# Kernel tuning notes

Hardware: AMD Instinct MI355X
Metric: run time of the kernel (lower is better)

The kernel has to match this reference:

```python
import jax, jax.numpy as jnp
import numpy as np

N, H, W, M = 1, 128, 128, 8
IN_CH, STYLE, VDIR, MASK, HID = 64, 128, 3, 680, 256


def setup_inputs() -> dict:
    key = jax.random.key(0)
    ks = iter(jax.random.split(key, 48))

    def rn(shape, scale=1.0):
        return jax.random.normal(next(ks), shape, jnp.float32) * scale

    d = {}
    d["x"] = rn((N, H, W, M, IN_CH))
    d["raydir"] = rn((N, H, W, 1, VDIR))
    d["z"] = rn((N, STYLE))
    d["m"] = jax.random.uniform(next(ks), (N, H, W, M, MASK), jnp.float32)
    d["fc_m_a_w"] = rn((HID, MASK), 1.0 / np.sqrt(MASK))
    d["fc_viewdir_w"] = rn((HID, VDIR), 1.0 / np.sqrt(VDIR))
    d["fc1_w"] = rn((HID, IN_CH), 1.0 / np.sqrt(IN_CH))
    d["fc1_b"] = jnp.zeros((HID,), jnp.float32)
    for name in ["fc2", "fc3", "fc4", "fc6"]:
        d[name + "_w"] = rn((HID, HID), 1.0 / np.sqrt(HID))
        d[name + "_wa"] = rn((HID, STYLE), 1.0 / np.sqrt(STYLE))
        d[name + "_ba"] = jnp.ones((HID,), jnp.float32)
        d[name + "_wb"] = rn((HID, STYLE), 1.0 / np.sqrt(STYLE))
        d[name + "_bb"] = jnp.zeros((HID,), jnp.float32)
    d["fc_sigma_w"] = rn((1, HID), 1.0 / np.sqrt(HID))
    d["fc_sigma_b"] = jnp.zeros((1,), jnp.float32)
    d["fc5_w"] = rn((HID, HID), 1.0 / np.sqrt(HID))
    d["mod5_wa"] = rn((HID, STYLE), 1.0 / np.sqrt(STYLE))
    d["mod5_ba"] = jnp.ones((HID,), jnp.float32)
    d["mod5_wb"] = rn((HID, STYLE), 1.0 / np.sqrt(STYLE))
    d["mod5_bb"] = jnp.zeros((HID,), jnp.float32)
    d["fc_out_c_w"] = rn((3, HID), 1.0 / np.sqrt(HID))
    d["fc_out_c_b"] = jnp.zeros((3,), jnp.float32)
    return d


def _act(v):
    # LeakyReLU(0.2)
    return jnp.where(v >= 0, v, 0.2 * v)


def _modlin(f, z, w, wa, ba, wb, bb):
    # ModLinear with bias=False, mod_bias=True, output_mode=True.
    # Torch materializes per-sample modulated weights w*alpha then baddbmm;
    # mathematically identical to scaling the input: y = (f*alpha) @ w.T + beta.
    alpha = z @ wa.T + ba  # (N, in)
    beta = z @ wb.T + bb   # (N, out)
    y = jnp.einsum('bhwmi,oi->bhwmo', f * alpha[:, None, None, None, :], w)
    return y + beta[:, None, None, None, :]


def reference(x, raydir, z, m, fc_m_a_w, fc_viewdir_w, fc1_w, fc1_b,
              fc2_w, fc2_wa, fc2_ba, fc2_wb, fc2_bb,
              fc3_w, fc3_wa, fc3_ba, fc3_wb, fc3_bb,
              fc4_w, fc4_wa, fc4_ba, fc4_wb, fc4_bb,
              fc_sigma_w, fc_sigma_b, fc5_w,
              mod5_wa, mod5_ba, mod5_wb, mod5_bb,
              fc6_w, fc6_wa, fc6_ba, fc6_wb, fc6_bb,
              fc_out_c_w, fc_out_c_b):
    f = jnp.einsum('bhwmi,oi->bhwmo', x, fc1_w) + fc1_b
    f = f + jnp.einsum('bhwmi,oi->bhwmo', m, fc_m_a_w)  # use_seg branch
    f = _act(f)
    f = _act(_modlin(f, z, fc2_w, fc2_wa, fc2_ba, fc2_wb, fc2_bb))
    f = _act(_modlin(f, z, fc3_w, fc3_wa, fc3_ba, fc3_wb, fc3_bb))
    f = _act(_modlin(f, z, fc4_w, fc4_wa, fc4_ba, fc4_wb, fc4_bb))
    sigma = jnp.einsum('bhwmi,oi->bhwmo', f, fc_sigma_w) + fc_sigma_b
    # viewdir branch: plain linear, add view-direction features, AffineMod
    f = jnp.einsum('bhwmi,oi->bhwmo', f, fc5_w)
    f = f + jnp.einsum('bhwvi,oi->bhwvo', raydir, fc_viewdir_w)  # broadcasts over M
    alpha5 = z @ mod5_wa.T + mod5_ba
    beta5 = z @ mod5_wb.T + mod5_bb
    f = _act(f * alpha5[:, None, None, None, :] + beta5[:, None, None, None, :])
    f = _act(_modlin(f, z, fc6_w, fc6_wa, fc6_ba, fc6_wb, fc6_bb))
    c = jnp.einsum('bhwmi,oi->bhwmo', f, fc_out_c_w) + fc_out_c_b
    return (sigma, c)
```

## Files before the change

### kernel.cpp

```cpp
#include <hip/hip_runtime.h>

#define US unsigned short

typedef short bf16x8 __attribute__((ext_vector_type(8)));
typedef float f32x4 __attribute__((ext_vector_type(4)));

__device__ __forceinline__ float b2f(US u) {
  union { unsigned u; float f; } x; x.u = ((unsigned)u) << 16; return x.f;
}
__device__ __forceinline__ US f2b(float f) {
  union { float f; unsigned u; } x; x.f = f;
  unsigned r = x.u + 0x7FFFu + ((x.u >> 16) & 1u);
  return (US)(r >> 16);
}
__device__ __forceinline__ float lk(float v) { return v >= 0.f ? v : 0.2f * v; }

__device__ __forceinline__ float ldin(const void* p, int i, int fl) {
  return fl ? ((const float*)p)[i] : b2f(((const US*)p)[i]);
}

#define O_W1 0
#define O_W2 393216
#define O_W3 524288
#define O_W4 655360
#define O_W5 786432
#define O_W6 917504
#define O_B2 1048576
#define O_B3 1049600
#define O_B4 1050624
#define O_B6 1051648
#define O_VD 1052672
#define O_A2 1056800
#define O_A3 1057824
#define O_A4 1058848
#define O_A6 1059872
#define O_A5 1060896
#define O_B5 1061920
#define O_FLAG 1062944

__global__ void detect_dtype(const void* x, char* ws) {
  if (threadIdx.x == 0) {
    const US* p = (const US*)x;
    int wild = 0;
    for (int i = 0; i < 512; ++i) {
      float v = b2f(p[i]);
      float a = fabsf(v);
      if (!(a <= 1e3f) || (a != 0.f && a < 1e-3f)) ++wild;
    }
    *(int*)(ws + O_FLAG) = (wild > 32) ? 1 : 0;
  }
}

struct S1Args {
  const void* z;
  const void* w[10];
  const void* b[10];
};

__global__ void setup_vec(S1Args a, char* ws) {
  const int outoff[10] = {O_A2, O_A3, O_A4, O_A6, O_B2, O_B3, O_B4, O_B6, O_A5, O_B5};
  int fl = *(const int*)(ws + O_FLAG);
  int v = blockIdx.x, k = threadIdx.x;
  const void* W = a.w[v];
  float acc = ldin(a.b[v], k, fl);
  for (int s = 0; s < 128; ++s) acc += ldin(a.z, s, fl) * ldin(W, k * 128 + s, fl);
  *(float*)(ws + outoff[v] + k * 4) = acc;
}

struct S2Args {
  const void *fc1_w, *fc1_b, *m_w, *w2, *w3, *w4, *w5, *w6, *vdw;
};

__global__ void setup_w(S2Args a, char* ws) {
  int fl = *(const int*)(ws + O_FLAG);
  int b = blockIdx.x, t = threadIdx.x;
  if (b < 256) {
    int n = b;
    US* W1p = (US*)(ws + O_W1);
    for (int i = 0; i < 3; ++i) {
      int k = t + i * 256;
      float v;
      if (k < 64) v = ldin(a.fc1_w, n * 64 + k, fl);
      else if (k < 744) v = ldin(a.m_w, n * 680 + k - 64, fl);
      else if (k == 744) v = ldin(a.fc1_b, n, fl);
      else v = 0.f;
      W1p[n * 768 + k] = f2b(v);
    }
  } else if (b < 1536) {
    int li = (b - 256) >> 8;
    int n = (b - 256) & 255;
    int k = t;
    const void* Wsrc = (li == 0) ? a.w2 : (li == 1) ? a.w3 : (li == 2) ? a.w4
                      : (li == 3) ? a.w5 : a.w6;
    const int aoff[5] = {O_A2, O_A3, O_A4, O_A5, O_A6};
    US* Wdst = (US*)(ws + O_W2 + li * 131072);
    float alpha = (li == 3) ? *(const float*)(ws + O_A5 + n * 4)
                            : *(const float*)(ws + aoff[li] + k * 4);
    Wdst[n * 256 + k] = f2b(ldin(Wsrc, n * 256 + k, fl) * alpha);
  } else {
    int n = t;
    float a5 = *(const float*)(ws + O_A5 + n * 4);
    float b5 = *(const float*)(ws + O_B5 + n * 4);
    float* vp = (float*)(ws + O_VD + n * 16);
    vp[0] = a5 * ldin(a.vdw, n * 3 + 0, fl);
    vp[1] = a5 * ldin(a.vdw, n * 3 + 1, fl);
    vp[2] = a5 * ldin(a.vdw, n * 3 + 2, fl);
    vp[3] = b5;
  }
}


#define FACT(r, c) (((r) << 8) + ((((c) ^ ((r) & 7))) << 3))
#define STG(buf, r, c) (16384 + ((buf) << 11) + ((r) << 5) + ((((c) ^ ((r) & 3))) << 3))

#define INITZERO() do { f32x4 zz = {0.f, 0.f, 0.f, 0.f};                      \
  _Pragma("unroll") for (int rt = 0; rt < 4; ++rt)                            \
  _Pragma("unroll") for (int nt = 0; nt < 4; ++nt) acc[rt][nt] = zz; } while (0)

#define INITBETA(OFF) do {                                                    \
  _Pragma("unroll") for (int nt = 0; nt < 4; ++nt) {                          \
    float bv = *(const float*)(ws + (OFF) + ((wave << 6) + (nt << 4) + l16) * 4); \
    f32x4 tt = {bv, bv, bv, bv};                                              \
    _Pragma("unroll") for (int rt = 0; rt < 4; ++rt) acc[rt][nt] = tt; } } while (0)

#define LAYER256(WP) do {                                                     \
  _Pragma("unroll 4") for (int ks = 0; ks < 8; ++ks) {                        \
    bf16x8 a[4];                                                              \
    _Pragma("unroll") for (int rt = 0; rt < 4; ++rt) {                        \
      int r = (rt << 4) + l16;                                                \
      a[rt] = *(const bf16x8*)&lds[FACT(r, (ks << 2) + q)];                   \
    }                                                                         \
    _Pragma("unroll") for (int nt = 0; nt < 4; ++nt) {                        \
      bf16x8 b = *(const bf16x8*)((WP) + ((wave << 6) + (nt << 4) + l16) * 256 + (ks << 5) + (q << 3)); \
      _Pragma("unroll") for (int rt = 0; rt < 4; ++rt)                        \
        acc[rt][nt] = __builtin_amdgcn_mfma_f32_16x16x32_bf16(a[rt], b, acc[rt][nt], 0, 0, 0); \
    }                                                                         \
  } } while (0)

#define EPIACT() do {                                                         \
  _Pragma("unroll") for (int nt = 0; nt < 4; ++nt) {                          \
    int k = (wave << 6) + (nt << 4) + l16;                                    \
    _Pragma("unroll") for (int rt = 0; rt < 4; ++rt)                          \
    _Pragma("unroll") for (int rg = 0; rg < 4; ++rg) {                        \
      int r = (rt << 4) + (q << 2) + rg;                                      \
      lds[FACT(r, k >> 3) + (k & 7)] = f2b(lk(acc[rt][nt][rg]));              \
    } }                                                                       \
  __syncthreads(); } while (0)

__device__ __forceinline__ bf16x8 loadA1(const void* __restrict__ x,
                                         const void* __restrict__ m,
                                         int fl, int g, int s, int skk) {
  int k = s * 32 + skk;
  bf16x8 v = {0, 0, 0, 0, 0, 0, 0, 0};
  if (k < 744) {
    if (fl) {
      const float* p = (k < 64) ? (const float*)x + g * 64 + k
                                : (const float*)m + g * 680 + (k - 64);
#pragma unroll
      for (int j = 0; j < 8; ++j) v[j] = (short)f2b(p[j]);
    } else {
      const US* p = (k < 64) ? (const US*)x + g * 64 + k
                             : (const US*)m + g * 680 + (k - 64);
      v = *(const bf16x8*)p;
    }
  } else if (k == 744) {
    v[0] = (short)0x3F80;
  }
  return v;
}

__global__ __launch_bounds__(256, 2) void mlp_main(
    const void* __restrict__ x, const void* __restrict__ rdir, const void* __restrict__ m,
    const void* __restrict__ wsig, const void* __restrict__ bsig,
    const void* __restrict__ wout, const void* __restrict__ bout,
    const char* __restrict__ ws, void* __restrict__ out) {
  __shared__ US lds[20480];
  const int fl = *(const int*)(ws + O_FLAG);
  const int tid = threadIdx.x;
  const int wave = tid >> 6, lane = tid & 63;
  const int l16 = lane & 15, q = lane >> 4;
  const int R0 = blockIdx.x * 64;

  const US* W1p = (const US*)(ws + O_W1);
  const US* W2p = (const US*)(ws + O_W2);
  const US* W3p = (const US*)(ws + O_W3);
  const US* W4p = (const US*)(ws + O_W4);
  const US* W5p = (const US*)(ws + O_W5);
  const US* W6p = (const US*)(ws + O_W6);

  f32x4 acc[4][4];

  INITZERO();
  {
    const int srow = tid >> 2, skk = (tid & 3) << 3, g = R0 + srow;
    bf16x8 cur = loadA1(x, m, fl, g, 0, skk);
    *(bf16x8*)&lds[STG(0, srow, skk >> 3)] = cur;
#pragma unroll 1
    for (int s = 0; s < 24; ++s) {
      bf16x8 nxt;
      if (s < 23) nxt = loadA1(x, m, fl, g, s + 1, skk);
      __syncthreads();
      bf16x8 a[4];
#pragma unroll
      for (int rt = 0; rt < 4; ++rt) {
        int r = (rt << 4) + l16;
        a[rt] = *(const bf16x8*)&lds[STG(s & 1, r, q)];
      }
#pragma unroll
      for (int nt = 0; nt < 4; ++nt) {
        bf16x8 b = *(const bf16x8*)(W1p + ((wave << 6) + (nt << 4) + l16) * 768 + (s << 5) + (q << 3));
#pragma unroll
        for (int rt = 0; rt < 4; ++rt)
          acc[rt][nt] = __builtin_amdgcn_mfma_f32_16x16x32_bf16(a[rt], b, acc[rt][nt], 0, 0, 0);
      }
      if (s < 23) *(bf16x8*)&lds[STG((s + 1) & 1, srow, skk >> 3)] = nxt;
    }
  }
  EPIACT();

  INITBETA(O_B2); LAYER256(W2p); __syncthreads(); EPIACT();
  INITBETA(O_B3); LAYER256(W3p); __syncthreads(); EPIACT();
  INITBETA(O_B4); LAYER256(W4p); __syncthreads(); EPIACT();

  {
    int r = tid >> 2, q4 = tid & 3, g = R0 + r;
    float sgv = 0.f;
#pragma unroll
    for (int i = 0; i < 8; ++i) {
      int c = q4 * 8 + i;
      bf16x8 av = *(const bf16x8*)&lds[FACT(r, c)];
#pragma unroll
      for (int j = 0; j < 8; ++j) sgv += b2f((US)av[j]) * ldin(wsig, c * 8 + j, fl);
    }
    sgv += __shfl_xor(sgv, 1);
    sgv += __shfl_xor(sgv, 2);
    if (q4 == 0) {
      float v = sgv + ldin(bsig, 0, fl);
      if (fl) ((float*)out)[g] = v; else ((US*)out)[g] = f2b(v);
    }
  }
  if (tid < 24) ((float*)&lds[16384])[tid] = ldin(rdir, (R0 >> 3) * 3 + tid, fl);

  INITZERO();
  LAYER256(W5p);
  __syncthreads();
  {
    const float* rays = (const float*)&lds[16384];
    float ry[4][3];
#pragma unroll
    for (int rt = 0; rt < 4; ++rt) {
      int p = rt * 2 + (q >> 1);
      ry[rt][0] = rays[p * 3 + 0]; ry[rt][1] = rays[p * 3 + 1]; ry[rt][2] = rays[p * 3 + 2];
    }
#pragma unroll
    for (int nt = 0; nt < 4; ++nt) {
      int n = (wave << 6) + (nt << 4) + l16;
      float4 vp = *(const float4*)(ws + O_VD + n * 16);
#pragma unroll
      for (int rt = 0; rt < 4; ++rt) {
#pragma unroll
        for (int rg = 0; rg < 4; ++rg) {
          float v = acc[rt][nt][rg] + ry[rt][0] * vp.x + ry[rt][1] * vp.y + ry[rt][2] * vp.z + vp.w;
          v = lk(v);
          int r = (rt << 4) + (q << 2) + rg;
          lds[FACT(r, n >> 3) + (n & 7)] = f2b(v);
        }
      }
    }
  }
  __syncthreads();

  INITBETA(O_B6); LAYER256(W6p); __syncthreads(); EPIACT();

  {
    int r = tid >> 2, q4 = tid & 3, g = R0 + r;
    float c0 = 0.f, c1 = 0.f, c2 = 0.f;
#pragma unroll
    for (int i = 0; i < 8; ++i) {
      int c = q4 * 8 + i;
      bf16x8 av = *(const bf16x8*)&lds[FACT(r, c)];
#pragma unroll
      for (int j = 0; j < 8; ++j) {
        float f = b2f((US)av[j]);
        int ci = c * 8 + j;
        c0 += f * ldin(wout, ci, fl);
        c1 += f * ldin(wout, 256 + ci, fl);
        c2 += f * ldin(wout, 512 + ci, fl);
      }
    }
    c0 += __shfl_xor(c0, 1); c0 += __shfl_xor(c0, 2);
    c1 += __shfl_xor(c1, 1); c1 += __shfl_xor(c1, 2);
    c2 += __shfl_xor(c2, 1); c2 += __shfl_xor(c2, 2);
    if (q4 == 0) {
      float v0 = c0 + ldin(bout, 0, fl);
      float v1 = c1 + ldin(bout, 1, fl);
      float v2 = c2 + ldin(bout, 2, fl);
      if (fl) {
        float* o = (float*)out + 131072 + g * 3;
        o[0] = v0; o[1] = v1; o[2] = v2;
      } else {
        US* o = (US*)out + 131072 + g * 3;
        o[0] = f2b(v0); o[1] = f2b(v1); o[2] = f2b(v2);
      }
    }
  }
}

extern "C" void kernel_launch(void* const* d_in, const int* in_sizes, int n_in,
                              void* d_out, int out_size, void* d_ws, size_t ws_size,
                              hipStream_t stream) {
  const void* in[37];
  for (int i = 0; i < 37 && i < n_in; ++i) in[i] = d_in[i];
  char* ws = (char*)d_ws;

  detect_dtype<<<1, 64, 0, stream>>>(in[0], ws);

  S1Args a1;
  a1.z = in[2];
  const int wi[10] = {9, 14, 19, 24, 11, 16, 21, 26, 31, 33};
  const int bi[10] = {10, 15, 20, 25, 12, 17, 22, 27, 32, 34};
  for (int i = 0; i < 10; ++i) { a1.w[i] = in[wi[i]]; a1.b[i] = in[bi[i]]; }
  setup_vec<<<10, 256, 0, stream>>>(a1, ws);

  S2Args a2{in[6], in[7], in[4], in[8], in[13], in[18], in[30], in[23], in[5]};
  setup_w<<<1537, 256, 0, stream>>>(a2, ws);

  mlp_main<<<2048, 256, 0, stream>>>(in[0], in[1], in[3], in[28], in[29], in[35], in[36],
                                     (const char*)ws, d_out);
}
```

Baseline: 885.4 us.

## Register double-buffer MLP operands, load layer-1 inputs directly, raise occupancy

Layer 1 no longer stages x/m through LDS with a barrier per k-step. Each wave now loads its A fragments straight from global memory, converting fp32 with packed bf16 instructions, and prefetches the next step's A and B into registers. The 256-wide layers get the same register double-buffering and raise MFMA issue priority with s_setprio. LDS shrinks and launch bounds go to 3 blocks per CU for more occupancy, and the dtype detection runs in parallel with a ballot. The risks are register pressure from the prefetch buffers at the higher occupancy target, and redundant global reads of x/m across the four waves.

```diff
diff --git a/kernel.cpp b/kernel.cpp
--- a/kernel.cpp
+++ b/kernel.cpp
@@ -14,6 +14,12 @@
   return (US)(r >> 16);
 }
 __device__ __forceinline__ float lk(float v) { return v >= 0.f ? v : 0.2f * v; }
+
+__device__ __forceinline__ unsigned cvtpk(float lo, float hi) {
+  unsigned r;
+  asm("v_cvt_pk_bf16_f32 %0, %1, %2" : "=v"(r) : "v"(lo), "v"(hi));
+  return r;
+}
 
 __device__ __forceinline__ float ldin(const void* p, int i, int fl) {
   return fl ? ((const float*)p)[i] : b2f(((const US*)p)[i]);
@@ -39,16 +45,17 @@
 #define O_FLAG 1062944
 
 __global__ void detect_dtype(const void* x, char* ws) {
-  if (threadIdx.x == 0) {
-    const US* p = (const US*)x;
-    int wild = 0;
-    for (int i = 0; i < 512; ++i) {
-      float v = b2f(p[i]);
-      float a = fabsf(v);
-      if (!(a <= 1e3f) || (a != 0.f && a < 1e-3f)) ++wild;
-    }
-    *(int*)(ws + O_FLAG) = (wild > 32) ? 1 : 0;
-  }
+  __shared__ int cnt;
+  if (threadIdx.x == 0) cnt = 0;
+  __syncthreads();
+  const US* p = (const US*)x;
+  float v = b2f(p[threadIdx.x]);
+  float a = fabsf(v);
+  int wild = (!(a <= 1e3f) || (a != 0.f && a < 1e-3f)) ? 1 : 0;
+  unsigned long long bal = __ballot(wild);
+  if ((threadIdx.x & 63) == 0) atomicAdd(&cnt, __popcll(bal));
+  __syncthreads();
+  if (threadIdx.x == 0) *(int*)(ws + O_FLAG) = (cnt > 32) ? 1 : 0;
 }
 
 struct S1Args {
@@ -111,7 +118,6 @@
 
 
 #define FACT(r, c) (((r) << 8) + ((((c) ^ ((r) & 7))) << 3))
-#define STG(buf, r, c) (16384 + ((buf) << 11) + ((r) << 5) + ((((c) ^ ((r) & 3))) << 3))
 
 #define INITZERO() do { f32x4 zz = {0.f, 0.f, 0.f, 0.f};                      \
   _Pragma("unroll") for (int rt = 0; rt < 4; ++rt)                            \
@@ -124,16 +130,27 @@
     _Pragma("unroll") for (int rt = 0; rt < 4; ++rt) acc[rt][nt] = tt; } } while (0)
 
 #define LAYER256(WP) do {                                                     \
-  _Pragma("unroll 4") for (int ks = 0; ks < 8; ++ks) {                        \
-    bf16x8 a[4];                                                              \
-    _Pragma("unroll") for (int rt = 0; rt < 4; ++rt) {                        \
-      int r = (rt << 4) + l16;                                                \
-      a[rt] = *(const bf16x8*)&lds[FACT(r, (ks << 2) + q)];                   \
+  bf16x8 aC[4], bC[4];                                                        \
+  _Pragma("unroll") for (int rt = 0; rt < 4; ++rt)                            \
+    aC[rt] = *(const bf16x8*)&lds[FACT((rt << 4) + l16, q)];                  \
+  _Pragma("unroll") for (int nt = 0; nt < 4; ++nt)                            \
+    bC[nt] = *(const bf16x8*)((WP) + ((wave << 6) + (nt << 4) + l16) * 256 + (q << 3)); \
+  _Pragma("unroll 2") for (int ks = 0; ks < 8; ++ks) {                        \
+    bf16x8 aN[4], bN[4];                                                      \
+    if (ks < 7) {                                                             \
+      _Pragma("unroll") for (int nt = 0; nt < 4; ++nt)                        \
+        bN[nt] = *(const bf16x8*)((WP) + ((wave << 6) + (nt << 4) + l16) * 256 + ((ks + 1) << 5) + (q << 3)); \
+      _Pragma("unroll") for (int rt = 0; rt < 4; ++rt)                        \
+        aN[rt] = *(const bf16x8*)&lds[FACT((rt << 4) + l16, ((ks + 1) << 2) + q)]; \
     }                                                                         \
-    _Pragma("unroll") for (int nt = 0; nt < 4; ++nt) {                        \
-      bf16x8 b = *(const bf16x8*)((WP) + ((wave << 6) + (nt << 4) + l16) * 256 + (ks << 5) + (q << 3)); \
+    __builtin_amdgcn_s_setprio(1);                                            \
+    _Pragma("unroll") for (int nt = 0; nt < 4; ++nt)                          \
       _Pragma("unroll") for (int rt = 0; rt < 4; ++rt)                        \
-        acc[rt][nt] = __builtin_amdgcn_mfma_f32_16x16x32_bf16(a[rt], b, acc[rt][nt], 0, 0, 0); \
+        acc[rt][nt] = __builtin_amdgcn_mfma_f32_16x16x32_bf16(aC[rt], bC[nt], acc[rt][nt], 0, 0, 0); \
+    __builtin_amdgcn_s_setprio(0);                                            \
+    if (ks < 7) {                                                             \
+      _Pragma("unroll") for (int rt = 0; rt < 4; ++rt) aC[rt] = aN[rt];       \
+      _Pragma("unroll") for (int nt = 0; nt < 4; ++nt) bC[nt] = bN[nt];       \
     }                                                                         \
   } } while (0)
 
@@ -147,34 +164,36 @@
     } }                                                                       \
   __syncthreads(); } while (0)
 
-__device__ __forceinline__ bf16x8 loadA1(const void* __restrict__ x,
-                                         const void* __restrict__ m,
-                                         int fl, int g, int s, int skk) {
-  int k = s * 32 + skk;
-  bf16x8 v = {0, 0, 0, 0, 0, 0, 0, 0};
+__device__ __forceinline__ bf16x8 loadA1d(const void* __restrict__ x,
+                                          const void* __restrict__ m,
+                                          int fl, int g, int k) {
+  union { bf16x8 v; unsigned u[4]; } r;
   if (k < 744) {
     if (fl) {
       const float* p = (k < 64) ? (const float*)x + g * 64 + k
                                 : (const float*)m + g * 680 + (k - 64);
-#pragma unroll
-      for (int j = 0; j < 8; ++j) v[j] = (short)f2b(p[j]);
+      float4 p0 = *(const float4*)p;
+      float4 p1 = *(const float4*)(p + 4);
+      r.u[0] = cvtpk(p0.x, p0.y); r.u[1] = cvtpk(p0.z, p0.w);
+      r.u[2] = cvtpk(p1.x, p1.y); r.u[3] = cvtpk(p1.z, p1.w);
     } else {
       const US* p = (k < 64) ? (const US*)x + g * 64 + k
                              : (const US*)m + g * 680 + (k - 64);
-      v = *(const bf16x8*)p;
-    }
-  } else if (k == 744) {
-    v[0] = (short)0x3F80;
-  }
-  return v;
-}
-
-__global__ __launch_bounds__(256, 2) void mlp_main(
+      r.v = *(const bf16x8*)p;
+    }
+  } else {
+    r.u[0] = (k == 744) ? 0x3F80u : 0u;
+    r.u[1] = 0; r.u[2] = 0; r.u[3] = 0;
+  }
+  return r.v;
+}
+
+__global__ __launch_bounds__(256, 3) void mlp_main(
     const void* __restrict__ x, const void* __restrict__ rdir, const void* __restrict__ m,
     const void* __restrict__ wsig, const void* __restrict__ bsig,
     const void* __restrict__ wout, const void* __restrict__ bout,
     const char* __restrict__ ws, void* __restrict__ out) {
-  __shared__ US lds[20480];
+  __shared__ US lds[16448];
   const int fl = *(const int*)(ws + O_FLAG);
   const int tid = threadIdx.x;
   const int wave = tid >> 6, lane = tid & 63;
@@ -192,28 +211,38 @@
 
   INITZERO();
   {
-    const int srow = tid >> 2, skk = (tid & 3) << 3, g = R0 + srow;
-    bf16x8 cur = loadA1(x, m, fl, g, 0, skk);
-    *(bf16x8*)&lds[STG(0, srow, skk >> 3)] = cur;
-#pragma unroll 1
+    const int kq = q << 3;
+    bf16x8 aC[4], bC[4];
+#pragma unroll
+    for (int nt = 0; nt < 4; ++nt)
+      bC[nt] = *(const bf16x8*)(W1p + ((wave << 6) + (nt << 4) + l16) * 768 + kq);
+#pragma unroll
+    for (int rt = 0; rt < 4; ++rt)
+      aC[rt] = loadA1d(x, m, fl, R0 + (rt << 4) + l16, kq);
+#pragma unroll 2
     for (int s = 0; s < 24; ++s) {
-      bf16x8 nxt;
-      if (s < 23) nxt = loadA1(x, m, fl, g, s + 1, skk);
-      __syncthreads();
-      bf16x8 a[4];
-#pragma unroll
-      for (int rt = 0; rt < 4; ++rt) {
-        int r = (rt << 4) + l16;
-        a[rt] = *(const bf16x8*)&lds[STG(s & 1, r, q)];
-      }
-#pragma unroll
-      for (int nt = 0; nt < 4; ++nt) {
-        bf16x8 b = *(const bf16x8*)(W1p + ((wave << 6) + (nt << 4) + l16) * 768 + (s << 5) + (q << 3));
+      bf16x8 aN[4], bN[4];
+      if (s < 23) {
+#pragma unroll
+        for (int nt = 0; nt < 4; ++nt)
+          bN[nt] = *(const bf16x8*)(W1p + ((wave << 6) + (nt << 4) + l16) * 768 + (s + 1) * 32 + kq);
 #pragma unroll
         for (int rt = 0; rt < 4; ++rt)
-          acc[rt][nt] = __builtin_amdgcn_mfma_f32_16x16x32_bf16(a[rt], b, acc[rt][nt], 0, 0, 0);
-      }
-      if (s < 23) *(bf16x8*)&lds[STG((s + 1) & 1, srow, skk >> 3)] = nxt;
+          aN[rt] = loadA1d(x, m, fl, R0 + (rt << 4) + l16, (s + 1) * 32 + kq);
+      }
+      __builtin_amdgcn_s_setprio(1);
+#pragma unroll
+      for (int nt = 0; nt < 4; ++nt)
+#pragma unroll
+        for (int rt = 0; rt < 4; ++rt)
+          acc[rt][nt] = __builtin_amdgcn_mfma_f32_16x16x32_bf16(aC[rt], bC[nt], acc[rt][nt], 0, 0, 0);
+      __builtin_amdgcn_s_setprio(0);
+      if (s < 23) {
+#pragma unroll
+        for (int rt = 0; rt < 4; ++rt) aC[rt] = aN[rt];
+#pragma unroll
+        for (int nt = 0; nt < 4; ++nt) bC[nt] = bN[nt];
+      }
     }
   }
   EPIACT();
@@ -313,7 +342,7 @@
   for (int i = 0; i < 37 && i < n_in; ++i) in[i] = d_in[i];
   char* ws = (char*)d_ws;
 
-  detect_dtype<<<1, 64, 0, stream>>>(in[0], ws);
+  detect_dtype<<<1, 512, 0, stream>>>(in[0], ws);
 
   S1Args a1;
   a1.z = in[2];
```

Result: slower. 1.200 ms (+35.5%).
